# Optimization experiments

Hardware: AMD Instinct MI355X
Metric: run time of the kernel (lower is better)

## Reference

```python
import jax, jax.numpy as jnp
import numpy as np

N, S, L, E, H = 8, 2, 512, 1024, 16
D = E // H  # head_dim = 64


def setup_inputs() -> dict:
    key = jax.random.key(0)
    ks = jax.random.split(key, 10)
    inp = {
        "values": jax.random.normal(ks[0], (N, S, L, E), dtype=jnp.float32),
        "keys": jax.random.normal(ks[1], (N, S, L, E), dtype=jnp.float32),
        "query": jax.random.normal(ks[2], (N, S, L, E), dtype=jnp.float32),
        "mask": jax.random.randint(ks[3], (N, S, L, 1), 0, 2, dtype=jnp.int32),
        # per-head projection weights, nn.Linear(D, D, bias=False): y = x @ W.T
        "Wv": jax.random.normal(ks[4], (D, D), dtype=jnp.float32) / np.sqrt(D),
        "Wk": jax.random.normal(ks[5], (D, D), dtype=jnp.float32) / np.sqrt(D),
        "Wq": jax.random.normal(ks[6], (D, D), dtype=jnp.float32) / np.sqrt(D),
        # output projection nn.Linear(E, E)
        "Wo": jax.random.normal(ks[7], (E, E), dtype=jnp.float32) / np.sqrt(E),
        "bo": jax.random.normal(ks[8], (E,), dtype=jnp.float32) * 0.01,
    }
    return inp


def reference(values, keys, query, mask, Wv, Wk, Wq, Wo, bo):
    n, s, l, e = query.shape
    h, d = H, D
    key_len = keys.shape[2]
    # split heads: (n, s, len, h, d)
    v = values.reshape(n, s, l, h, d) @ Wv.T
    k = keys.reshape(n, s, l, h, d) @ Wk.T
    q = query.reshape(n, s, l, h, d) @ Wq.T
    # energy: (n, s, h, q_len, k_len)
    energy = jnp.einsum('nsqhd,nskhd->nshqk', q, k)
    # mask[:, :, :, 0] masks QUERY positions (broadcast over heads and k)
    m = mask[:, :, :, 0]  # (n, s, l)
    energy = jnp.where(m[:, :, None, :, None] == 0, jnp.float32(-1e20), energy)
    # NOTE: softmax over the QUERY axis (dim=3), faithful to the original
    attn = jax.nn.softmax(energy / jnp.sqrt(jnp.float32(key_len)), axis=3)
    out = jnp.einsum('nshql,nslhd->nsqhd', attn, v)
    out = out.reshape(n, s, l, h * d)
    return out @ Wo.T + bo
```

## Files before the change

### kernel.cpp

```cpp
#include <hip/hip_runtime.h>
#include <math.h>

#define LL 512
#define EE 1024
#define HH 16
#define DD 64
#define NSX 16
#define NT (NSX*LL)
#define NSLE (NT*EE)
#define SCALE_Q 0.06375871f

typedef unsigned short u16;
typedef short bf16x8 __attribute__((ext_vector_type(8)));
typedef float f32x4 __attribute__((ext_vector_type(4)));

__device__ inline u16 f2bf(float f) {
  unsigned u = __float_as_uint(f);
  u += 0x7fff + ((u >> 16) & 1);
  return (u16)(u >> 16);
}

#define FEXP2(x) __builtin_amdgcn_exp2f(x)
#define MFMA32(a, b, c) __builtin_amdgcn_mfma_f32_16x16x32_bf16((a), (b), (c), 0, 0, 0)

__device__ inline void gload16(const void* g, void* l) {
  __builtin_amdgcn_global_load_lds(
      (const __attribute__((address_space(1))) unsigned int*)g,
      (__attribute__((address_space(3))) unsigned int*)l, 16, 0, 0);
}

__global__ void __launch_bounds__(256) convw_kernel(
    const float* __restrict__ Wv, const float* __restrict__ Wk,
    const float* __restrict__ Wq, const float* __restrict__ Wo,
    u16* __restrict__ Wvb, u16* __restrict__ Wkb,
    u16* __restrict__ Wqb, u16* __restrict__ Wob) {
  int i = blockIdx.x * 256 + threadIdx.x;
  const float* s; u16* d; int j;
  if (i < 262144) { s = Wo; d = Wob; j = i; }
  else {
    j = i - 262144;
    if (j < 1024)      { s = Wv; d = Wvb; }
    else if (j < 2048) { s = Wk; d = Wkb; j -= 1024; }
    else               { s = Wq; d = Wqb; j -= 2048; }
  }
  float4 f = ((const float4*)s)[j];
  ushort4 o; o.x = f2bf(f.x); o.y = f2bf(f.y); o.z = f2bf(f.z); o.w = f2bf(f.w);
  ((ushort4*)d)[j] = o;
}

__global__ void __launch_bounds__(256) proj_kernel(
    const float* __restrict__ vals, const float* __restrict__ keys,
    const float* __restrict__ qry,
    const u16* __restrict__ Wvb, const u16* __restrict__ Wkb,
    const u16* __restrict__ Wqb,
    u16* __restrict__ vpT, u16* __restrict__ kp, u16* __restrict__ qp) {
  const int b = blockIdx.x;
  const int tt0 = b & 7, hg = (b >> 3) & 3, ns = (b >> 5) & 15, mat = b >> 9;
  const int tid = threadIdx.x;
  const int wid = tid >> 6, lane = tid & 63, quad = lane >> 4, l16 = lane & 15;
  const int h = hg*4 + wid;
  const float* src = (mat == 0 ? vals : mat == 1 ? keys : qry);
  const u16*   W   = (mat == 0 ? Wvb  : mat == 1 ? Wkb  : Wqb);
  u16* dst = (mat == 1 ? kp : qp);
  const float sc = (mat == 2) ? SCALE_Q : 1.f;
  bf16x8 wf[4][2];
  #pragma unroll
  for (int nt = 0; nt < 4; ++nt) {
    wf[nt][0] = *(const bf16x8*)&W[(nt*16 + l16)*DD + quad*8];
    wf[nt][1] = *(const bf16x8*)&W[(nt*16 + l16)*DD + 32 + quad*8];
  }
  f32x4 z = {0.f, 0.f, 0.f, 0.f};
  const float* xr0 = src + (size_t)(ns*LL + tt0*16 + l16)*EE + h*DD;
  const float* xr1 = xr0 + (size_t)128*EE;
  float4 x0 = *(const float4*)&xr0[quad*8];
  float4 x1 = *(const float4*)&xr0[quad*8 + 4];
  float4 x2 = *(const float4*)&xr0[32 + quad*8];
  float4 x3 = *(const float4*)&xr0[32 + quad*8 + 4];
  float4 y0 = *(const float4*)&xr1[quad*8];
  float4 y1 = *(const float4*)&xr1[quad*8 + 4];
  float4 y2 = *(const float4*)&xr1[32 + quad*8];
  float4 y3 = *(const float4*)&xr1[32 + quad*8 + 4];
  #pragma unroll
  for (int j = 0; j < 4; ++j) {
    const int tt = tt0 + 8*j;
    const int t0 = ns*LL + tt*16;
    float4 n0, n1, n2, n3;
    if (j < 2) {
      const float* xrn = src + (size_t)(t0 + 256 + l16)*EE + h*DD;
      n0 = *(const float4*)&xrn[quad*8];
      n1 = *(const float4*)&xrn[quad*8 + 4];
      n2 = *(const float4*)&xrn[32 + quad*8];
      n3 = *(const float4*)&xrn[32 + quad*8 + 4];
    }
    bf16x8 af0, af1;
    af0[0] = (short)f2bf(x0.x); af0[1] = (short)f2bf(x0.y);
    af0[2] = (short)f2bf(x0.z); af0[3] = (short)f2bf(x0.w);
    af0[4] = (short)f2bf(x1.x); af0[5] = (short)f2bf(x1.y);
    af0[6] = (short)f2bf(x1.z); af0[7] = (short)f2bf(x1.w);
    af1[0] = (short)f2bf(x2.x); af1[1] = (short)f2bf(x2.y);
    af1[2] = (short)f2bf(x2.z); af1[3] = (short)f2bf(x2.w);
    af1[4] = (short)f2bf(x3.x); af1[5] = (short)f2bf(x3.y);
    af1[6] = (short)f2bf(x3.z); af1[7] = (short)f2bf(x3.w);
    if (mat == 0) {
      f32x4 acc[4];
      #pragma unroll
      for (int nt = 0; nt < 4; ++nt) {
        acc[nt] = MFMA32(af0, wf[nt][0], z);
        acc[nt] = MFMA32(af1, wf[nt][1], acc[nt]);
      }
      #pragma unroll
      for (int nt = 0; nt < 4; ++nt) {
        ushort4 o;
        o.x = f2bf(acc[nt][0]); o.y = f2bf(acc[nt][1]);
        o.z = f2bf(acc[nt][2]); o.w = f2bf(acc[nt][3]);
        size_t idx = ((size_t)((ns*HH + h)*DD + nt*16 + l16))*LL + tt*16 + quad*4;
        *(ushort4*)&vpT[idx] = o;
      }
    } else {
      f32x4 acc[4];
      #pragma unroll
      for (int nt = 0; nt < 4; ++nt) {
        acc[nt] = MFMA32(wf[nt][0], af0, z);
        acc[nt] = MFMA32(wf[nt][1], af1, acc[nt]);
      }
      #pragma unroll
      for (int nt = 0; nt < 4; ++nt) {
        ushort4 o;
        o.x = f2bf(acc[nt][0] * sc); o.y = f2bf(acc[nt][1] * sc);
        o.z = f2bf(acc[nt][2] * sc); o.w = f2bf(acc[nt][3] * sc);
        *(ushort4*)&dst[(size_t)(t0 + l16)*EE + h*DD + nt*16 + quad*4] = o;
      }
    }
    x0 = y0; x1 = y1; x2 = y2; x3 = y3;
    if (j < 2) { y0 = n0; y1 = n1; y2 = n2; y3 = n3; }
  }
}

__global__ void __launch_bounds__(1024, 4) attn_kernel(
    const u16* __restrict__ qp, const u16* __restrict__ kp,
    const u16* __restrict__ vpT, const int* __restrict__ mask,
    u16* __restrict__ oat) {
  const int b = blockIdx.x;
  const int h = b & 15, ns = b >> 4;
  const int tid = threadIdx.x;
  const int wid = tid >> 6, lane = tid & 63, quad = lane >> 4, l16 = lane & 15;
  __shared__ u16 Ks[LL][72];
  __shared__ u16 Vt[2][DD][72];
  __shared__ u16 pt[16][32][40];
  __shared__ float csum[LL];
  float* psum = (float*)pt;
  const size_t kgbase = ((size_t)(ns*LL))*EE + h*DD;
  for (int i = tid; i < 4096; i += 1024) {
    int row = i >> 3, seg = (i & 7) * 8;
    *(bf16x8*)&Ks[row][seg] = *(const bf16x8*)&kp[kgbase + (size_t)row*EE + seg];
  }
  const int q0 = wid*32;
  bf16x8 qf[2][2];
  float maf[2][4];
  float mqf[2];
  #pragma unroll
  for (int qt = 0; qt < 2; ++qt) {
    const u16* qrow = qp + ((size_t)(ns*LL + q0 + qt*16 + l16))*EE + h*DD;
    qf[qt][0] = *(const bf16x8*)&qrow[quad*8];
    qf[qt][1] = *(const bf16x8*)&qrow[32 + quad*8];
    #pragma unroll
    for (int r = 0; r < 4; ++r)
      maf[qt][r] = mask[ns*LL + q0 + qt*16 + quad*4 + r] ? 1.f : 0.f;
    mqf[qt] = mask[ns*LL + q0 + qt*16 + l16] ? 1.f : 0.f;
  }
  f32x4 z = {0.f, 0.f, 0.f, 0.f};
  __syncthreads();
  for (int lt = 0; lt < 32; ++lt) {
    bf16x8 kf0 = *(const bf16x8*)&Ks[lt*16 + l16][quad*8];
    bf16x8 kf1 = *(const bf16x8*)&Ks[lt*16 + l16][32 + quad*8];
    float part = 0.f;
    #pragma unroll
    for (int qt = 0; qt < 2; ++qt) {
      f32x4 e = MFMA32(qf[qt][0], kf0, z);
      e = MFMA32(qf[qt][1], kf1, e);
      #pragma unroll
      for (int r = 0; r < 4; ++r)
        part += maf[qt][r] * FEXP2(e[r]);
    }
    part += __shfl_xor(part, 16);
    part += __shfl_xor(part, 32);
    if (quad == 0) psum[wid*512 + lt*16 + l16] = part;
  }
  __syncthreads();
  if (tid < LL) {
    float s = 0.f;
    #pragma unroll
    for (int w = 0; w < 16; ++w) s += psum[w*512 + tid];
    csum[tid] = (s > 0.f) ? 1.f/s : 0.f;
  }
  __syncthreads();
  f32x4 acc[4][2] = {{z,z},{z,z},{z,z},{z,z}};
  const size_t vgbase = ((size_t)((ns*HH + h)*DD))*LL;
  for (int lc = 0; lc < 8; ++lc) {
    if (tid < 512) {
      int row = tid >> 3, seg = (tid & 7) * 8;
      *(bf16x8*)&Vt[lc & 1][row][seg] =
          *(const bf16x8*)&vpT[vgbase + (size_t)row*LL + lc*64 + seg];
    }
    __syncthreads();
    #pragma unroll
    for (int lt2 = 0; lt2 < 4; ++lt2) {
      const int lb = lc*64 + lt2*16;
      bf16x8 kf0 = *(const bf16x8*)&Ks[lb + l16][quad*8];
      bf16x8 kf1 = *(const bf16x8*)&Ks[lb + l16][32 + quad*8];
      float4 cs4 = *(const float4*)&csum[lb + quad*4];
      #pragma unroll
      for (int qt = 0; qt < 2; ++qt) {
        f32x4 e = MFMA32(kf0, qf[qt][0], z);
        e = MFMA32(kf1, qf[qt][1], e);
        const float m = mqf[qt];
        ushort4 o;
        o.x = f2bf(m * cs4.x * FEXP2(e[0]));
        o.y = f2bf(m * cs4.y * FEXP2(e[1]));
        o.z = f2bf(m * cs4.z * FEXP2(e[2]));
        o.w = f2bf(m * cs4.w * FEXP2(e[3]));
        *(ushort4*)&pt[wid][qt*16 + l16][(lt2 & 1)*16 + quad*4] = o;
        if (lt2 & 1) {
          bf16x8 pa = *(const bf16x8*)&pt[wid][qt*16 + l16][quad*8];
          #pragma unroll
          for (int dt = 0; dt < 4; ++dt) {
            bf16x8 vb = *(const bf16x8*)&Vt[lc & 1][dt*16 + l16]
                                        [(lt2 >> 1)*32 + quad*8];
            acc[dt][qt] = MFMA32(pa, vb, acc[dt][qt]);
          }
        }
      }
    }
  }
  #pragma unroll
  for (int qt = 0; qt < 2; ++qt)
    #pragma unroll
    for (int dt = 0; dt < 4; ++dt)
      #pragma unroll
      for (int r = 0; r < 4; ++r)
        oat[((size_t)(ns*LL + q0 + qt*16 + quad*4 + r))*EE + h*DD + dt*16 + l16] =
            f2bf(acc[dt][qt][r]);
}

__global__ void __launch_bounds__(256) out_gemm_kernel(
    const u16* __restrict__ A, const u16* __restrict__ Wob,
    const float* __restrict__ bo, float* __restrict__ Y) {
  __shared__ u16 As[128][64];
  __shared__ u16 Bs[64][64];
  const int b = blockIdx.x;
  const int nb = b & 15, mb = b >> 4;
  const int m0 = mb*128, n0 = nb*64;
  const int tid = threadIdx.x;
  const int wid = tid >> 6, lane = tid & 63, quad = lane >> 4, l16 = lane & 15;
  const int wm = (wid >> 1)*64, wn = (wid & 1)*32;
  const int r0 = tid >> 3, sseg = (tid & 7) * 8;
  u16* adst = &As[0][0] + tid*8;
  u16* bdst = &Bs[0][0] + tid*8;
  f32x4 z = {0.f, 0.f, 0.f, 0.f};
  f32x4 acc[4][2];
  #pragma unroll
  for (int i = 0; i < 4; ++i)
    #pragma unroll
    for (int j = 0; j < 2; ++j) acc[i][j] = z;
  for (int k0 = 0; k0 < EE; k0 += 64) {
    __syncthreads();
    #pragma unroll
    for (int it = 0; it < 4; ++it)
      gload16(&A[(size_t)(m0 + it*32 + r0)*EE + k0 + sseg], adst + it*2048);
    #pragma unroll
    for (int it = 0; it < 2; ++it)
      gload16(&Wob[(size_t)(n0 + it*32 + r0)*EE + k0 + sseg], bdst + it*2048);
    __syncthreads();
    #pragma unroll
    for (int kk = 0; kk < 2; ++kk) {
      bf16x8 af[4], bfr[2];
      #pragma unroll
      for (int i = 0; i < 4; ++i)
        af[i] = *(const bf16x8*)&As[wm + i*16 + l16][kk*32 + quad*8];
      #pragma unroll
      for (int j = 0; j < 2; ++j)
        bfr[j] = *(const bf16x8*)&Bs[wn + j*16 + l16][kk*32 + quad*8];
      #pragma unroll
      for (int i = 0; i < 4; ++i)
        #pragma unroll
        for (int j = 0; j < 2; ++j)
          acc[i][j] = MFMA32(af[i], bfr[j], acc[i][j]);
    }
  }
  #pragma unroll
  for (int i = 0; i < 4; ++i)
    #pragma unroll
    for (int j = 0; j < 2; ++j) {
      int col = n0 + wn + j*16 + l16;
      float bias = bo[col];
      #pragma unroll
      for (int r = 0; r < 4; ++r)
        Y[(size_t)(m0 + wm + i*16 + quad*4 + r)*EE + col] = acc[i][j][r] + bias;
    }
}

extern "C" void kernel_launch(void* const* d_in, const int* in_sizes, int n_in,
                              void* d_out, int out_size, void* d_ws, size_t ws_size,
                              hipStream_t stream) {
  const float* values = (const float*)d_in[0];
  const float* keysp  = (const float*)d_in[1];
  const float* query  = (const float*)d_in[2];
  const int*   mask   = (const int*)d_in[3];
  const float* Wv = (const float*)d_in[4];
  const float* Wk = (const float*)d_in[5];
  const float* Wq = (const float*)d_in[6];
  const float* Wo = (const float*)d_in[7];
  const float* bo = (const float*)d_in[8];
  float* Y = (float*)d_out;

  u16* qp  = (u16*)d_ws;
  u16* kp  = qp + NSLE;
  u16* vpT = kp + NSLE;
  u16* oat = vpT + NSLE;
  u16* Wob = oat + NSLE;
  u16* Wvb = Wob + EE*EE;
  u16* Wkb = Wvb + DD*DD;
  u16* Wqb = Wkb + DD*DD;

  convw_kernel<<<1036, 256, 0, stream>>>(Wv, Wk, Wq, Wo, Wvb, Wkb, Wqb, Wob);
  proj_kernel<<<3*NSX*4*8, 256, 0, stream>>>(values, keysp, query,
                                             Wvb, Wkb, Wqb, vpT, kp, qp);
  attn_kernel<<<NSX*HH, 1024, 0, stream>>>(qp, kp, vpT, mask, oat);
  out_gemm_kernel<<<(NT/128)*(EE/64), 256, 0, stream>>>(oat, Wob, bo, Y);
}
```

Measured before the change: 230.7 us.

## Split attention into column-sum and PV kernels with atomic reduction for more blocks

Splits the single 1024-thread-per-(ns,h) attention kernel into two kernels. The first computes per-key column sums across query tiles and reduces them with global atomicAdd into a buffer that the weight-conversion kernel now zeroes. The second normalizes and performs P·V over 128-query slices. This raises block count from 256 to 2048 and 1024 blocks of 256 threads, improving CU occupancy and removing the large shared K tile. The cost is that K is read from global memory twice, a float atomic reduction is added, and there is one extra launch.

```diff
diff --git a/kernel.cpp b/kernel.cpp
--- a/kernel.cpp
+++ b/kernel.cpp
@@ -33,7 +33,8 @@
     const float* __restrict__ Wv, const float* __restrict__ Wk,
     const float* __restrict__ Wq, const float* __restrict__ Wo,
     u16* __restrict__ Wvb, u16* __restrict__ Wkb,
-    u16* __restrict__ Wqb, u16* __restrict__ Wob) {
+    u16* __restrict__ Wqb, u16* __restrict__ Wob,
+    float* __restrict__ csum) {
   int i = blockIdx.x * 256 + threadIdx.x;
   const float* s; u16* d; int j;
   if (i < 262144) { s = Wo; d = Wob; j = i; }
@@ -41,7 +42,12 @@
     j = i - 262144;
     if (j < 1024)      { s = Wv; d = Wvb; }
     else if (j < 2048) { s = Wk; d = Wkb; j -= 1024; }
-    else               { s = Wq; d = Wqb; j -= 2048; }
+    else if (j < 3072) { s = Wq; d = Wqb; j -= 2048; }
+    else {
+      float4 zz = {0.f, 0.f, 0.f, 0.f};
+      ((float4*)csum)[j - 3072] = zz;
+      return;
+    }
   }
   float4 f = ((const float4*)s)[j];
   ushort4 o; o.x = f2bf(f.x); o.y = f2bf(f.y); o.z = f2bf(f.z); o.w = f2bf(f.w);
@@ -136,28 +142,16 @@
   }
 }
 
-__global__ void __launch_bounds__(1024, 4) attn_kernel(
+__global__ void __launch_bounds__(256) attn_cs_kernel(
     const u16* __restrict__ qp, const u16* __restrict__ kp,
-    const u16* __restrict__ vpT, const int* __restrict__ mask,
-    u16* __restrict__ oat) {
+    const int* __restrict__ mask, float* __restrict__ csum) {
   const int b = blockIdx.x;
-  const int h = b & 15, ns = b >> 4;
+  const int ls = b & 1, qs = (b >> 1) & 3, h = (b >> 3) & 15, ns = b >> 7;
   const int tid = threadIdx.x;
   const int wid = tid >> 6, lane = tid & 63, quad = lane >> 4, l16 = lane & 15;
-  __shared__ u16 Ks[LL][72];
-  __shared__ u16 Vt[2][DD][72];
-  __shared__ u16 pt[16][32][40];
-  __shared__ float csum[LL];
-  float* psum = (float*)pt;
-  const size_t kgbase = ((size_t)(ns*LL))*EE + h*DD;
-  for (int i = tid; i < 4096; i += 1024) {
-    int row = i >> 3, seg = (i & 7) * 8;
-    *(bf16x8*)&Ks[row][seg] = *(const bf16x8*)&kp[kgbase + (size_t)row*EE + seg];
-  }
-  const int q0 = wid*32;
+  const int q0 = qs*128 + wid*32;
   bf16x8 qf[2][2];
   float maf[2][4];
-  float mqf[2];
   #pragma unroll
   for (int qt = 0; qt < 2; ++qt) {
     const u16* qrow = qp + ((size_t)(ns*LL + q0 + qt*16 + l16))*EE + h*DD;
@@ -166,13 +160,15 @@
     #pragma unroll
     for (int r = 0; r < 4; ++r)
       maf[qt][r] = mask[ns*LL + q0 + qt*16 + quad*4 + r] ? 1.f : 0.f;
-    mqf[qt] = mask[ns*LL + q0 + qt*16 + l16] ? 1.f : 0.f;
   }
   f32x4 z = {0.f, 0.f, 0.f, 0.f};
-  __syncthreads();
-  for (int lt = 0; lt < 32; ++lt) {
-    bf16x8 kf0 = *(const bf16x8*)&Ks[lt*16 + l16][quad*8];
-    bf16x8 kf1 = *(const bf16x8*)&Ks[lt*16 + l16][32 + quad*8];
+  const u16* kbase = kp + ((size_t)(ns*LL + ls*256))*EE + h*DD;
+  float* cbase = csum + (ns*HH + h)*LL + ls*256;
+  #pragma unroll 4
+  for (int lt = 0; lt < 16; ++lt) {
+    const u16* krow = kbase + (size_t)(lt*16 + l16)*EE;
+    bf16x8 kf0 = *(const bf16x8*)&krow[quad*8];
+    bf16x8 kf1 = *(const bf16x8*)&krow[32 + quad*8];
     float part = 0.f;
     #pragma unroll
     for (int qt = 0; qt < 2; ++qt) {
@@ -184,31 +180,56 @@
     }
     part += __shfl_xor(part, 16);
     part += __shfl_xor(part, 32);
-    if (quad == 0) psum[wid*512 + lt*16 + l16] = part;
-  }
-  __syncthreads();
-  if (tid < LL) {
-    float s = 0.f;
-    #pragma unroll
-    for (int w = 0; w < 16; ++w) s += psum[w*512 + tid];
-    csum[tid] = (s > 0.f) ? 1.f/s : 0.f;
-  }
-  __syncthreads();
+    if (quad == 0) atomicAdd(&cbase[lt*16 + l16], part);
+  }
+}
+
+__global__ void __launch_bounds__(256) attn_pv_kernel(
+    const u16* __restrict__ qp, const u16* __restrict__ kp,
+    const u16* __restrict__ vpT, const int* __restrict__ mask,
+    const float* __restrict__ csum, u16* __restrict__ oat) {
+  const int b = blockIdx.x;
+  const int qs = b & 3, h = (b >> 2) & 15, ns = b >> 6;
+  const int tid = threadIdx.x;
+  const int wid = tid >> 6, lane = tid & 63, quad = lane >> 4, l16 = lane & 15;
+  __shared__ u16 Vt[2][DD][72];
+  __shared__ u16 pt[4][32][40];
+  __shared__ float csinv[LL];
+  const float* cbase = csum + (ns*HH + h)*LL;
+  for (int i = tid; i < LL; i += 256) {
+    float s = cbase[i];
+    csinv[i] = (s > 0.f) ? 1.f/s : 0.f;
+  }
+  const int q0 = qs*128 + wid*32;
+  bf16x8 qf[2][2];
+  float mqf[2];
+  #pragma unroll
+  for (int qt = 0; qt < 2; ++qt) {
+    const u16* qrow = qp + ((size_t)(ns*LL + q0 + qt*16 + l16))*EE + h*DD;
+    qf[qt][0] = *(const bf16x8*)&qrow[quad*8];
+    qf[qt][1] = *(const bf16x8*)&qrow[32 + quad*8];
+    mqf[qt] = mask[ns*LL + q0 + qt*16 + l16] ? 1.f : 0.f;
+  }
+  f32x4 z = {0.f, 0.f, 0.f, 0.f};
   f32x4 acc[4][2] = {{z,z},{z,z},{z,z},{z,z}};
   const size_t vgbase = ((size_t)((ns*HH + h)*DD))*LL;
+  const u16* kbase = kp + ((size_t)(ns*LL))*EE + h*DD;
+  __syncthreads();
   for (int lc = 0; lc < 8; ++lc) {
-    if (tid < 512) {
-      int row = tid >> 3, seg = (tid & 7) * 8;
-      *(bf16x8*)&Vt[lc & 1][row][seg] =
-          *(const bf16x8*)&vpT[vgbase + (size_t)row*LL + lc*64 + seg];
+    {
+      int row = tid >> 2, seg = (tid & 3) * 16;
+      const u16* vsrc = &vpT[vgbase + (size_t)row*LL + lc*64 + seg];
+      *(bf16x8*)&Vt[lc & 1][row][seg]     = *(const bf16x8*)&vsrc[0];
+      *(bf16x8*)&Vt[lc & 1][row][seg + 8] = *(const bf16x8*)&vsrc[8];
     }
     __syncthreads();
     #pragma unroll
     for (int lt2 = 0; lt2 < 4; ++lt2) {
       const int lb = lc*64 + lt2*16;
-      bf16x8 kf0 = *(const bf16x8*)&Ks[lb + l16][quad*8];
-      bf16x8 kf1 = *(const bf16x8*)&Ks[lb + l16][32 + quad*8];
-      float4 cs4 = *(const float4*)&csum[lb + quad*4];
+      const u16* krow = kbase + (size_t)(lb + l16)*EE;
+      bf16x8 kf0 = *(const bf16x8*)&krow[quad*8];
+      bf16x8 kf1 = *(const bf16x8*)&krow[32 + quad*8];
+      float4 cs4 = *(const float4*)&csinv[lb + quad*4];
       #pragma unroll
       for (int qt = 0; qt < 2; ++qt) {
         f32x4 e = MFMA32(kf0, qf[qt][0], z);
@@ -220,14 +241,19 @@
         o.z = f2bf(m * cs4.z * FEXP2(e[2]));
         o.w = f2bf(m * cs4.w * FEXP2(e[3]));
         *(ushort4*)&pt[wid][qt*16 + l16][(lt2 & 1)*16 + quad*4] = o;
-        if (lt2 & 1) {
+      }
+      if (lt2 & 1) {
+        bf16x8 vb[4];
+        #pragma unroll
+        for (int dt = 0; dt < 4; ++dt)
+          vb[dt] = *(const bf16x8*)&Vt[lc & 1][dt*16 + l16]
+                                      [(lt2 >> 1)*32 + quad*8];
+        #pragma unroll
+        for (int qt = 0; qt < 2; ++qt) {
           bf16x8 pa = *(const bf16x8*)&pt[wid][qt*16 + l16][quad*8];
           #pragma unroll
-          for (int dt = 0; dt < 4; ++dt) {
-            bf16x8 vb = *(const bf16x8*)&Vt[lc & 1][dt*16 + l16]
-                                        [(lt2 >> 1)*32 + quad*8];
-            acc[dt][qt] = MFMA32(pa, vb, acc[dt][qt]);
-          }
+          for (int dt = 0; dt < 4; ++dt)
+            acc[dt][qt] = MFMA32(pa, vb[dt], acc[dt][qt]);
         }
       }
     }
@@ -321,10 +347,13 @@
   u16* Wvb = Wob + EE*EE;
   u16* Wkb = Wvb + DD*DD;
   u16* Wqb = Wkb + DD*DD;
-
-  convw_kernel<<<1036, 256, 0, stream>>>(Wv, Wk, Wq, Wo, Wvb, Wkb, Wqb, Wob);
+  float* csum = (float*)(Wqb + DD*DD);
+
+  convw_kernel<<<1164, 256, 0, stream>>>(Wv, Wk, Wq, Wo, Wvb, Wkb, Wqb, Wob,
+                                         csum);
   proj_kernel<<<3*NSX*4*8, 256, 0, stream>>>(values, keysp, query,
                                              Wvb, Wkb, Wqb, vpT, kp, qp);
-  attn_kernel<<<NSX*HH, 1024, 0, stream>>>(qp, kp, vpT, mask, oat);
+  attn_cs_kernel<<<NSX*HH*8, 256, 0, stream>>>(qp, kp, mask, csum);
+  attn_pv_kernel<<<NSX*HH*4, 256, 0, stream>>>(qp, kp, vpT, mask, csum, oat);
   out_gemm_kernel<<<(NT/128)*(EE/64), 256, 0, stream>>>(oat, Wob, bo, Y);
 }
```

New measurement: 268.1 us. 1.16x slower.

## Register-prefetch V tiles in attention and hoist all projection input loads

Applied to the files above, without the earlier changes.

In the projection kernel, all four row-tile input loads are issued up front into a register array, replacing the rolling two-stage prefetch. In the attention kernel, V tiles are now loaded by all 1024 threads into registers one chunk ahead and written to the double-buffered shared tile after compute. This hides global load latency behind the MFMA work. The V fragments are also read from shared memory once per step and reused across both query tiles, which cuts LDS traffic but raises register pressure under the 1024-thread launch bound.

```diff
diff --git a/kernel.cpp b/kernel.cpp
--- a/kernel.cpp
+++ b/kernel.cpp
@@ -63,6 +63,15 @@
   const u16*   W   = (mat == 0 ? Wvb  : mat == 1 ? Wkb  : Wqb);
   u16* dst = (mat == 1 ? kp : qp);
   const float sc = (mat == 2) ? SCALE_Q : 1.f;
+  float4 x[4][4];
+  #pragma unroll
+  for (int j = 0; j < 4; ++j) {
+    const float* xr = src + (size_t)(ns*LL + (tt0 + 8*j)*16 + l16)*EE + h*DD;
+    x[j][0] = *(const float4*)&xr[quad*8];
+    x[j][1] = *(const float4*)&xr[quad*8 + 4];
+    x[j][2] = *(const float4*)&xr[32 + quad*8];
+    x[j][3] = *(const float4*)&xr[32 + quad*8 + 4];
+  }
   bf16x8 wf[4][2];
   #pragma unroll
   for (int nt = 0; nt < 4; ++nt) {
@@ -70,37 +79,19 @@
     wf[nt][1] = *(const bf16x8*)&W[(nt*16 + l16)*DD + 32 + quad*8];
   }
   f32x4 z = {0.f, 0.f, 0.f, 0.f};
-  const float* xr0 = src + (size_t)(ns*LL + tt0*16 + l16)*EE + h*DD;
-  const float* xr1 = xr0 + (size_t)128*EE;
-  float4 x0 = *(const float4*)&xr0[quad*8];
-  float4 x1 = *(const float4*)&xr0[quad*8 + 4];
-  float4 x2 = *(const float4*)&xr0[32 + quad*8];
-  float4 x3 = *(const float4*)&xr0[32 + quad*8 + 4];
-  float4 y0 = *(const float4*)&xr1[quad*8];
-  float4 y1 = *(const float4*)&xr1[quad*8 + 4];
-  float4 y2 = *(const float4*)&xr1[32 + quad*8];
-  float4 y3 = *(const float4*)&xr1[32 + quad*8 + 4];
   #pragma unroll
   for (int j = 0; j < 4; ++j) {
     const int tt = tt0 + 8*j;
     const int t0 = ns*LL + tt*16;
-    float4 n0, n1, n2, n3;
-    if (j < 2) {
-      const float* xrn = src + (size_t)(t0 + 256 + l16)*EE + h*DD;
-      n0 = *(const float4*)&xrn[quad*8];
-      n1 = *(const float4*)&xrn[quad*8 + 4];
-      n2 = *(const float4*)&xrn[32 + quad*8];
-      n3 = *(const float4*)&xrn[32 + quad*8 + 4];
-    }
     bf16x8 af0, af1;
-    af0[0] = (short)f2bf(x0.x); af0[1] = (short)f2bf(x0.y);
-    af0[2] = (short)f2bf(x0.z); af0[3] = (short)f2bf(x0.w);
-    af0[4] = (short)f2bf(x1.x); af0[5] = (short)f2bf(x1.y);
-    af0[6] = (short)f2bf(x1.z); af0[7] = (short)f2bf(x1.w);
-    af1[0] = (short)f2bf(x2.x); af1[1] = (short)f2bf(x2.y);
-    af1[2] = (short)f2bf(x2.z); af1[3] = (short)f2bf(x2.w);
-    af1[4] = (short)f2bf(x3.x); af1[5] = (short)f2bf(x3.y);
-    af1[6] = (short)f2bf(x3.z); af1[7] = (short)f2bf(x3.w);
+    af0[0] = (short)f2bf(x[j][0].x); af0[1] = (short)f2bf(x[j][0].y);
+    af0[2] = (short)f2bf(x[j][0].z); af0[3] = (short)f2bf(x[j][0].w);
+    af0[4] = (short)f2bf(x[j][1].x); af0[5] = (short)f2bf(x[j][1].y);
+    af0[6] = (short)f2bf(x[j][1].z); af0[7] = (short)f2bf(x[j][1].w);
+    af1[0] = (short)f2bf(x[j][2].x); af1[1] = (short)f2bf(x[j][2].y);
+    af1[2] = (short)f2bf(x[j][2].z); af1[3] = (short)f2bf(x[j][2].w);
+    af1[4] = (short)f2bf(x[j][3].x); af1[5] = (short)f2bf(x[j][3].y);
+    af1[6] = (short)f2bf(x[j][3].z); af1[7] = (short)f2bf(x[j][3].w);
     if (mat == 0) {
       f32x4 acc[4];
       #pragma unroll
@@ -131,8 +122,6 @@
         *(ushort4*)&dst[(size_t)(t0 + l16)*EE + h*DD + nt*16 + quad*4] = o;
       }
     }
-    x0 = y0; x1 = y1; x2 = y2; x3 = y3;
-    if (j < 2) { y0 = n0; y1 = n1; y2 = n2; y3 = n3; }
   }
 }
 
@@ -149,6 +138,9 @@
   __shared__ u16 pt[16][32][40];
   __shared__ float csum[LL];
   float* psum = (float*)pt;
+  const size_t vgbase = ((size_t)((ns*HH + h)*DD))*LL;
+  const int vrow = tid >> 4, vseg = (tid & 15) * 4;
+  ushort4 vreg = *(const ushort4*)&vpT[vgbase + (size_t)vrow*LL + vseg];
   const size_t kgbase = ((size_t)(ns*LL))*EE + h*DD;
   for (int i = tid; i < 4096; i += 1024) {
     int row = i >> 3, seg = (i & 7) * 8;
@@ -194,14 +186,12 @@
     csum[tid] = (s > 0.f) ? 1.f/s : 0.f;
   }
   __syncthreads();
+  *(ushort4*)&Vt[0][vrow][vseg] = vreg;
   f32x4 acc[4][2] = {{z,z},{z,z},{z,z},{z,z}};
-  const size_t vgbase = ((size_t)((ns*HH + h)*DD))*LL;
   for (int lc = 0; lc < 8; ++lc) {
-    if (tid < 512) {
-      int row = tid >> 3, seg = (tid & 7) * 8;
-      *(bf16x8*)&Vt[lc & 1][row][seg] =
-          *(const bf16x8*)&vpT[vgbase + (size_t)row*LL + lc*64 + seg];
-    }
+    ushort4 nreg;
+    if (lc < 7)
+      nreg = *(const ushort4*)&vpT[vgbase + (size_t)vrow*LL + (lc+1)*64 + vseg];
     __syncthreads();
     #pragma unroll
     for (int lt2 = 0; lt2 < 4; ++lt2) {
@@ -220,17 +210,24 @@
         o.z = f2bf(m * cs4.z * FEXP2(e[2]));
         o.w = f2bf(m * cs4.w * FEXP2(e[3]));
         *(ushort4*)&pt[wid][qt*16 + l16][(lt2 & 1)*16 + quad*4] = o;
-        if (lt2 & 1) {
+      }
+      if (lt2 & 1) {
+        bf16x8 vb[4];
+        #pragma unroll
+        for (int dt = 0; dt < 4; ++dt)
+          vb[dt] = *(const bf16x8*)&Vt[lc & 1][dt*16 + l16]
+                                      [(lt2 >> 1)*32 + quad*8];
+        #pragma unroll
+        for (int qt = 0; qt < 2; ++qt) {
           bf16x8 pa = *(const bf16x8*)&pt[wid][qt*16 + l16][quad*8];
           #pragma unroll
-          for (int dt = 0; dt < 4; ++dt) {
-            bf16x8 vb = *(const bf16x8*)&Vt[lc & 1][dt*16 + l16]
-                                        [(lt2 >> 1)*32 + quad*8];
-            acc[dt][qt] = MFMA32(pa, vb, acc[dt][qt]);
-          }
+          for (int dt = 0; dt < 4; ++dt)
+            acc[dt][qt] = MFMA32(pa, vb[dt], acc[dt][qt]);
         }
       }
     }
+    if (lc < 7)
+      *(ushort4*)&Vt[(lc+1) & 1][vrow][vseg] = nreg;
   }
   #pragma unroll
   for (int qt = 0; qt < 2; ++qt)
```

Measured after the change: 232.8 us. No clear change (+0.9%).

## Fold weight conversion into projection kernel and stage V in two halves

Applied to the files above, without the earlier changes.

Removes the separate weight-conversion launch. The per-head weights are now converted to bf16 inside each projection block, and the Wo conversion runs as extra blocks of the projection kernel. In the attention kernel, the per-64-column V tile loop with a barrier per chunk is replaced by two 256-column halves. V is prefetched into registers early and written to LDS during the softmax-normalisation phase, which cuts the number of barriers. The cost is redundant weight conversion in every projection block and more LDS and register use for V.

```diff
diff --git a/kernel.cpp b/kernel.cpp
--- a/kernel.cpp
+++ b/kernel.cpp
@@ -20,6 +20,15 @@
   return (u16)(u >> 16);
 }
 
+__device__ inline bf16x8 pack8(float4 a, float4 b) {
+  bf16x8 r;
+  r[0] = (short)f2bf(a.x); r[1] = (short)f2bf(a.y);
+  r[2] = (short)f2bf(a.z); r[3] = (short)f2bf(a.w);
+  r[4] = (short)f2bf(b.x); r[5] = (short)f2bf(b.y);
+  r[6] = (short)f2bf(b.z); r[7] = (short)f2bf(b.w);
+  return r;
+}
+
 #define FEXP2(x) __builtin_amdgcn_exp2f(x)
 #define MFMA32(a, b, c) __builtin_amdgcn_mfma_f32_16x16x32_bf16((a), (b), (c), 0, 0, 0)
 
@@ -29,45 +38,36 @@
       (__attribute__((address_space(3))) unsigned int*)l, 16, 0, 0);
 }
 
-__global__ void __launch_bounds__(256) convw_kernel(
-    const float* __restrict__ Wv, const float* __restrict__ Wk,
-    const float* __restrict__ Wq, const float* __restrict__ Wo,
-    u16* __restrict__ Wvb, u16* __restrict__ Wkb,
-    u16* __restrict__ Wqb, u16* __restrict__ Wob) {
-  int i = blockIdx.x * 256 + threadIdx.x;
-  const float* s; u16* d; int j;
-  if (i < 262144) { s = Wo; d = Wob; j = i; }
-  else {
-    j = i - 262144;
-    if (j < 1024)      { s = Wv; d = Wvb; }
-    else if (j < 2048) { s = Wk; d = Wkb; j -= 1024; }
-    else               { s = Wq; d = Wqb; j -= 2048; }
-  }
-  float4 f = ((const float4*)s)[j];
-  ushort4 o; o.x = f2bf(f.x); o.y = f2bf(f.y); o.z = f2bf(f.z); o.w = f2bf(f.w);
-  ((ushort4*)d)[j] = o;
-}
-
 __global__ void __launch_bounds__(256) proj_kernel(
     const float* __restrict__ vals, const float* __restrict__ keys,
     const float* __restrict__ qry,
-    const u16* __restrict__ Wvb, const u16* __restrict__ Wkb,
-    const u16* __restrict__ Wqb,
-    u16* __restrict__ vpT, u16* __restrict__ kp, u16* __restrict__ qp) {
+    const float* __restrict__ Wv, const float* __restrict__ Wk,
+    const float* __restrict__ Wq, const float* __restrict__ Wo,
+    u16* __restrict__ vpT, u16* __restrict__ kp, u16* __restrict__ qp,
+    u16* __restrict__ Wob) {
   const int b = blockIdx.x;
+  const int tid = threadIdx.x;
+  if (b >= 1536) {
+    int i = (b - 1536)*256 + tid;
+    float4 f = ((const float4*)Wo)[i];
+    ushort4 o; o.x = f2bf(f.x); o.y = f2bf(f.y);
+    o.z = f2bf(f.z); o.w = f2bf(f.w);
+    ((ushort4*)Wob)[i] = o;
+    return;
+  }
   const int tt0 = b & 7, hg = (b >> 3) & 3, ns = (b >> 5) & 15, mat = b >> 9;
-  const int tid = threadIdx.x;
   const int wid = tid >> 6, lane = tid & 63, quad = lane >> 4, l16 = lane & 15;
   const int h = hg*4 + wid;
   const float* src = (mat == 0 ? vals : mat == 1 ? keys : qry);
-  const u16*   W   = (mat == 0 ? Wvb  : mat == 1 ? Wkb  : Wqb);
+  const float* Wf  = (mat == 0 ? Wv   : mat == 1 ? Wk   : Wq);
   u16* dst = (mat == 1 ? kp : qp);
   const float sc = (mat == 2) ? SCALE_Q : 1.f;
   bf16x8 wf[4][2];
   #pragma unroll
   for (int nt = 0; nt < 4; ++nt) {
-    wf[nt][0] = *(const bf16x8*)&W[(nt*16 + l16)*DD + quad*8];
-    wf[nt][1] = *(const bf16x8*)&W[(nt*16 + l16)*DD + 32 + quad*8];
+    const float* wr = Wf + (nt*16 + l16)*DD + quad*8;
+    wf[nt][0] = pack8(*(const float4*)&wr[0],  *(const float4*)&wr[4]);
+    wf[nt][1] = pack8(*(const float4*)&wr[32], *(const float4*)&wr[36]);
   }
   f32x4 z = {0.f, 0.f, 0.f, 0.f};
   const float* xr0 = src + (size_t)(ns*LL + tt0*16 + l16)*EE + h*DD;
@@ -92,15 +92,8 @@
       n2 = *(const float4*)&xrn[32 + quad*8];
       n3 = *(const float4*)&xrn[32 + quad*8 + 4];
     }
-    bf16x8 af0, af1;
-    af0[0] = (short)f2bf(x0.x); af0[1] = (short)f2bf(x0.y);
-    af0[2] = (short)f2bf(x0.z); af0[3] = (short)f2bf(x0.w);
-    af0[4] = (short)f2bf(x1.x); af0[5] = (short)f2bf(x1.y);
-    af0[6] = (short)f2bf(x1.z); af0[7] = (short)f2bf(x1.w);
-    af1[0] = (short)f2bf(x2.x); af1[1] = (short)f2bf(x2.y);
-    af1[2] = (short)f2bf(x2.z); af1[3] = (short)f2bf(x2.w);
-    af1[4] = (short)f2bf(x3.x); af1[5] = (short)f2bf(x3.y);
-    af1[6] = (short)f2bf(x3.z); af1[7] = (short)f2bf(x3.w);
+    bf16x8 af0 = pack8(x0, x1);
+    bf16x8 af1 = pack8(x2, x3);
     if (mat == 0) {
       f32x4 acc[4];
       #pragma unroll
@@ -145,10 +138,14 @@
   const int tid = threadIdx.x;
   const int wid = tid >> 6, lane = tid & 63, quad = lane >> 4, l16 = lane & 15;
   __shared__ u16 Ks[LL][72];
-  __shared__ u16 Vt[2][DD][72];
+  __shared__ u16 Vh[DD][260];
   __shared__ u16 pt[16][32][40];
   __shared__ float csum[LL];
   float* psum = (float*)pt;
+  const size_t vgbase = ((size_t)((ns*HH + h)*DD))*LL;
+  const int vrow = tid >> 4, vcol = (tid & 15) * 16;
+  bf16x8 v0a = *(const bf16x8*)&vpT[vgbase + (size_t)vrow*LL + vcol];
+  bf16x8 v0b = *(const bf16x8*)&vpT[vgbase + (size_t)vrow*LL + vcol + 8];
   const size_t kgbase = ((size_t)(ns*LL))*EE + h*DD;
   for (int i = tid; i < 4096; i += 1024) {
     int row = i >> 3, seg = (i & 7) * 8;
@@ -193,22 +190,20 @@
     for (int w = 0; w < 16; ++w) s += psum[w*512 + tid];
     csum[tid] = (s > 0.f) ? 1.f/s : 0.f;
   }
+  *(bf16x8*)&Vh[vrow][vcol]     = v0a;
+  *(bf16x8*)&Vh[vrow][vcol + 8] = v0b;
+  bf16x8 v1a = *(const bf16x8*)&vpT[vgbase + (size_t)vrow*LL + 256 + vcol];
+  bf16x8 v1b = *(const bf16x8*)&vpT[vgbase + (size_t)vrow*LL + 256 + vcol + 8];
   __syncthreads();
   f32x4 acc[4][2] = {{z,z},{z,z},{z,z},{z,z}};
-  const size_t vgbase = ((size_t)((ns*HH + h)*DD))*LL;
-  for (int lc = 0; lc < 8; ++lc) {
-    if (tid < 512) {
-      int row = tid >> 3, seg = (tid & 7) * 8;
-      *(bf16x8*)&Vt[lc & 1][row][seg] =
-          *(const bf16x8*)&vpT[vgbase + (size_t)row*LL + lc*64 + seg];
-    }
-    __syncthreads();
-    #pragma unroll
-    for (int lt2 = 0; lt2 < 4; ++lt2) {
-      const int lb = lc*64 + lt2*16;
-      bf16x8 kf0 = *(const bf16x8*)&Ks[lb + l16][quad*8];
-      bf16x8 kf1 = *(const bf16x8*)&Ks[lb + l16][32 + quad*8];
-      float4 cs4 = *(const float4*)&csum[lb + quad*4];
+  #pragma unroll
+  for (int half = 0; half < 2; ++half) {
+    #pragma unroll
+    for (int lt = 0; lt < 16; ++lt) {
+      const int labs = half*256 + lt*16;
+      bf16x8 kf0 = *(const bf16x8*)&Ks[labs + l16][quad*8];
+      bf16x8 kf1 = *(const bf16x8*)&Ks[labs + l16][32 + quad*8];
+      float4 cs4 = *(const float4*)&csum[labs + quad*4];
       #pragma unroll
       for (int qt = 0; qt < 2; ++qt) {
         f32x4 e = MFMA32(kf0, qf[qt][0], z);
@@ -219,17 +214,27 @@
         o.y = f2bf(m * cs4.y * FEXP2(e[1]));
         o.z = f2bf(m * cs4.z * FEXP2(e[2]));
         o.w = f2bf(m * cs4.w * FEXP2(e[3]));
-        *(ushort4*)&pt[wid][qt*16 + l16][(lt2 & 1)*16 + quad*4] = o;
-        if (lt2 & 1) {
+        *(ushort4*)&pt[wid][qt*16 + l16][(lt & 1)*16 + quad*4] = o;
+      }
+      if (lt & 1) {
+        bf16x8 vb[4];
+        #pragma unroll
+        for (int dt = 0; dt < 4; ++dt)
+          vb[dt] = *(const bf16x8*)&Vh[dt*16 + l16][(lt >> 1)*32 + quad*8];
+        #pragma unroll
+        for (int qt = 0; qt < 2; ++qt) {
           bf16x8 pa = *(const bf16x8*)&pt[wid][qt*16 + l16][quad*8];
           #pragma unroll
-          for (int dt = 0; dt < 4; ++dt) {
-            bf16x8 vb = *(const bf16x8*)&Vt[lc & 1][dt*16 + l16]
-                                        [(lt2 >> 1)*32 + quad*8];
-            acc[dt][qt] = MFMA32(pa, vb, acc[dt][qt]);
-          }
+          for (int dt = 0; dt < 4; ++dt)
+            acc[dt][qt] = MFMA32(pa, vb[dt], acc[dt][qt]);
         }
       }
+    }
+    if (half == 0) {
+      __syncthreads();
+      *(bf16x8*)&Vh[vrow][vcol]     = v1a;
+      *(bf16x8*)&Vh[vrow][vcol + 8] = v1b;
+      __syncthreads();
     }
   }
   #pragma unroll
@@ -318,13 +323,10 @@
   u16* vpT = kp + NSLE;
   u16* oat = vpT + NSLE;
   u16* Wob = oat + NSLE;
-  u16* Wvb = Wob + EE*EE;
-  u16* Wkb = Wvb + DD*DD;
-  u16* Wqb = Wkb + DD*DD;
-
-  convw_kernel<<<1036, 256, 0, stream>>>(Wv, Wk, Wq, Wo, Wvb, Wkb, Wqb, Wob);
-  proj_kernel<<<3*NSX*4*8, 256, 0, stream>>>(values, keysp, query,
-                                             Wvb, Wkb, Wqb, vpT, kp, qp);
+
+  proj_kernel<<<1536 + 1024, 256, 0, stream>>>(values, keysp, query,
+                                               Wv, Wk, Wq, Wo,
+                                               vpT, kp, qp, Wob);
   attn_kernel<<<NSX*HH, 1024, 0, stream>>>(qp, kp, vpT, mask, oat);
   out_gemm_kernel<<<(NT/128)*(EE/64), 256, 0, stream>>>(oat, Wob, bo, Y);
 }
```

Result: no change. 234.0 us (+1.4%).
